# Optimization experiments

Hardware: AMD Instinct MI355X
Metric: run time of the kernel (lower is better)

The kernel has to match this reference:

```python
import jax, jax.numpy as jnp
import numpy as np

B, C, H, N = 4, 128, 4, 2048
D = C // H  # head_dim = 32
BN_EPS = 1e-5


def _conv1(w, b, x):
    # 1x1 Conv1d: [O,C] x [B,C,N] -> [B,O,N]
    return jnp.einsum('oc,bcn->bon', w, x) + b[None, :, None]


def setup_inputs() -> dict:
    key = jax.random.key(0)
    ks = jax.random.split(key, 20)
    p = lambda k, shape: jax.random.normal(k, shape, dtype=jnp.float32) * 0.05
    return {
        'x1': jax.random.normal(ks[0], (B, C, N), dtype=jnp.float32),
        'x2': jax.random.normal(ks[1], (B, C, N), dtype=jnp.float32),
        'kv_mask': jnp.ones((B, N), dtype=bool),
        'wq': p(ks[2], (C, C)), 'bq': p(ks[3], (C,)),
        'wk': p(ks[4], (C, C)), 'bk': p(ks[5], (C,)),
        'wv': p(ks[6], (C, C)), 'bv': p(ks[7], (C,)),
        'wm': p(ks[8], (C, C)), 'bm': p(ks[9], (C,)),
        'wc1': p(ks[10], (2 * C, 2 * C)), 'bc1': p(ks[11], (2 * C,)),
        'bn_gamma': jnp.ones((2 * C,), dtype=jnp.float32),
        'bn_beta': jnp.zeros((2 * C,), dtype=jnp.float32),
        'bn_mean': p(ks[12], (2 * C,)),
        'bn_var': jax.random.uniform(ks[13], (2 * C,), dtype=jnp.float32, minval=0.5, maxval=1.5),
        'wc2': p(ks[14], (C, 2 * C)), 'bc2': p(ks[15], (C,)),
    }


def reference(x1, x2, kv_mask, wq, bq, wk, bk, wv, bv, wm, bm,
              wc1, bc1, bn_gamma, bn_beta, bn_mean, bn_var, wc2, bc2):
    b, _, n = x1.shape
    q = _conv1(wq, bq, x1).reshape(b, H, D, n)   # bhdn
    k = _conv1(wk, bk, x2).reshape(b, H, D, -1)  # bhdm
    v = _conv1(wv, bv, x2).reshape(b, H, D, -1)  # bhdm
    qk = jnp.einsum('bhdn,bhdm->bhnm', q, k)
    # masked_fill on raw QK before scaling, matching torch code
    qk = jnp.where(kv_mask[:, None, None, :], qk, jnp.float32(-1e6))
    score = jax.nn.softmax(qk * (1.0 / D ** 0.5), axis=-1)
    add_value = jnp.einsum('bhnm,bhdm->bhdn', score, v).reshape(b, C, n)
    add_value = _conv1(wm, bm, add_value)
    cat = jnp.concatenate([x1, add_value], axis=1)  # [B, 2C, N]
    h = _conv1(wc1, bc1, cat)
    # BatchNorm1d in inference mode (running stats)
    h = (h - bn_mean[None, :, None]) * jax.lax.rsqrt(bn_var[None, :, None] + BN_EPS)
    h = h * bn_gamma[None, :, None] + bn_beta[None, :, None]
    h = jax.nn.relu(h)
    h = _conv1(wc2, bc2, h)
    return x1 + h
```

## Files before the change

### kernel.cpp

```cpp
#include <hip/hip_runtime.h>

typedef __attribute__((ext_vector_type(4))) float v4f;
typedef __attribute__((ext_vector_type(8))) _Float16 half8;
typedef __attribute__((ext_vector_type(4))) _Float16 half4;
typedef __attribute__((ext_vector_type(2))) _Float16 half2t;

constexpr float C2 = 0.17677669529663687f * 1.44269504088896341f;

__device__ __forceinline__ half4 pk4(float a, float b, float c, float d) {
  half2t lo = __builtin_bit_cast(half2t, __builtin_amdgcn_cvt_pkrtz(a, b));
  half2t hi = __builtin_bit_cast(half2t, __builtin_amdgcn_cvt_pkrtz(c, d));
  return __builtin_shufflevector(lo, hi, 0, 1, 2, 3);
}

__global__ __launch_bounds__(256) void prep(
    const float* __restrict__ x1, const float* __restrict__ x2,
    const float* __restrict__ wq, const float* __restrict__ bq,
    const float* __restrict__ wk, const float* __restrict__ wv,
    const float* __restrict__ wm, const float* __restrict__ wc1,
    const float* __restrict__ wc2, const float* __restrict__ gamma,
    const float* __restrict__ beta, const float* __restrict__ mean,
    const float* __restrict__ var, const unsigned char* __restrict__ mask,
    _Float16* __restrict__ x1pk, _Float16* __restrict__ x2pk,
    _Float16* __restrict__ wts, float* __restrict__ bqs,
    float* __restrict__ A1, float* __restrict__ B1,
    float* __restrict__ maskf) {
  const int id = blockIdx.x * 256 + threadIdx.x;
  if (id < 524288) {
    const int u = id & 262143;
    const float* __restrict__ src = (id < 262144) ? x1 : x2;
    _Float16* __restrict__ dst = (id < 262144) ? x1pk : x2pk;
    const int n = u & 2047, r = u >> 11;
    const int q = r & 3, ct = (r >> 2) & 7, b = r >> 5;
    const float* s = src + ((size_t)(b * 128 + ct * 16 + q * 4) * 2048 + n);
    const half4 v = pk4(s[0], s[2048], s[4096], s[6144]);
    *(half4*)(dst + ((size_t)(b * 8 + ct) * 2048 + n) * 16 + q * 4) = v;
  } else if (id < 565248) {
    const int e = (id - 524288) * 4;
    const float* src;
    int base;
    float sc = 1.0f;
    if (e < 16384) { src = wq; base = 0; sc = C2; }
    else if (e < 32768) { src = wk; base = 16384; }
    else if (e < 49152) { src = wv; base = 32768; }
    else if (e < 65536) { src = wm; base = 49152; }
    else if (e < 131072) { src = wc1; base = 65536; }
    else { src = wc2; base = 131072; }
    const float4 t = *(const float4*)(src + (e - base));
    *(half4*)(wts + e) = pk4(t.x * sc, t.y * sc, t.z * sc, t.w * sc);
  } else if (id < 565312) {
    const int i = (id - 565248) * 4;
#pragma unroll
    for (int j = 0; j < 4; ++j) {
      const int oi = i + j;
      const float sc = gamma[oi] * rsqrtf(var[oi] + 1e-5f);
      A1[oi] = sc;
      B1[oi] = beta[oi] - mean[oi] * sc;
    }
  } else if (id < 565344) {
    const int i = (id - 565312) * 4;
#pragma unroll
    for (int j = 0; j < 4; ++j) bqs[i + j] = bq[i + j] * C2;
  } else if (id < 567392) {
    const int i = (id - 565344) * 4;
#pragma unroll
    for (int j = 0; j < 4; ++j)
      maskf[i + j] = mask[i + j] ? 0.0f : (-1.0e6f * C2);
  }
}

__global__ __launch_bounds__(512) void qkv(
    const _Float16* __restrict__ x1pk, const _Float16* __restrict__ x2pk,
    const _Float16* __restrict__ wts, const float* __restrict__ bqs,
    const float* __restrict__ bk, const float* __restrict__ bv,
    _Float16* __restrict__ Qpk, _Float16* __restrict__ Kpk,
    _Float16* __restrict__ Vpk) {
  const int b = blockIdx.y;
  const int bx = blockIdx.x;
  const int tid = threadIdx.x, w = tid >> 6, lane = tid & 63;
  const int l = lane & 15, q = lane >> 4;
  const int n = bx * 16 + l;
  const size_t xoff = ((size_t)(b * 8 + (q >> 1)) * 2048 + n) * 16 + (q & 1) * 8;

  half8 x1f[4], x2f[4];
#pragma unroll
  for (int kt = 0; kt < 4; ++kt) {
    x1f[kt] = *(const half8*)(x1pk + xoff + (size_t)kt * 2 * 2048 * 16);
    x2f[kt] = *(const half8*)(x2pk + xoff + (size_t)kt * 2 * 2048 * 16);
  }
  const _Float16* wq_h = wts;
  const _Float16* wk_h = wts + 16384;
  const _Float16* wv_h = wts + 32768;

#pragma unroll
  for (int i = 0; i < 3; ++i) {
    const int t = w * 3 + i;
    if (t < 8) {
      const int mt = t;
      v4f acc = *(const v4f*)(bqs + mt * 16 + q * 4);
#pragma unroll
      for (int kt = 0; kt < 4; ++kt) {
        const half8 wf =
            *(const half8*)(wq_h + (mt * 16 + l) * 128 + kt * 32 + q * 8);
        acc = __builtin_amdgcn_mfma_f32_16x16x32_f16(wf, x1f[kt], acc, 0, 0, 0);
      }
      *(half4*)(Qpk + ((size_t)(b * 8 + mt) * 2048 + n) * 16 + q * 4) =
          pk4(acc[0], acc[1], acc[2], acc[3]);
    } else if (t < 16) {
      const int mt = t - 8;
      v4f acc = *(const v4f*)(bk + mt * 16 + q * 4);
#pragma unroll
      for (int kt = 0; kt < 4; ++kt) {
        const half8 wf =
            *(const half8*)(wk_h + (mt * 16 + l) * 128 + kt * 32 + q * 8);
        acc = __builtin_amdgcn_mfma_f32_16x16x32_f16(wf, x2f[kt], acc, 0, 0, 0);
      }
      *(half4*)(Kpk + ((size_t)(b * 8 + mt) * 2048 + n) * 16 + q * 4) =
          pk4(acc[0], acc[1], acc[2], acc[3]);
    } else {
      const int ot = t - 16;
      const float bvv = bv[ot * 16 + l];
      v4f acc = {bvv, bvv, bvv, bvv};
#pragma unroll
      for (int kt = 0; kt < 4; ++kt) {
        const half8 wf =
            *(const half8*)(wv_h + (ot * 16 + l) * 128 + kt * 32 + q * 8);
        acc = __builtin_amdgcn_mfma_f32_16x16x32_f16(x2f[kt], wf, acc, 0, 0, 0);
      }
      *(half4*)(Vpk + (((size_t)(b * 4 + (ot >> 1)) * 128 + bx) * 32 +
                       (ot & 1) * 16 + l) * 16 + q * 4) =
          pk4(acc[0], acc[1], acc[2], acc[3]);
    }
  }
}

__global__ __launch_bounds__(256) void attn(
    const _Float16* __restrict__ Qpk, const _Float16* __restrict__ Kpk,
    const _Float16* __restrict__ Vpk, const float* __restrict__ maskf,
    _Float16* __restrict__ Opk, float* __restrict__ lsump) {
  const int bh = blockIdx.y, b = bh >> 2, h = bh & 3;
  const int n0 = blockIdx.x * 64;
  const int part = blockIdx.z;
  const int tid = threadIdx.x, w = tid >> 6, lane = tid & 63;
  const int l = lane & 15, q = lane >> 4;
  const int n = n0 + w * 16 + l;

  const half8 qf = *(const half8*)(
      Qpk + ((size_t)(b * 8 + h * 2 + (q >> 1)) * 2048 + n) * 16 + (q & 1) * 8);
  const _Float16* __restrict__ Kb =
      Kpk + ((size_t)(b * 8 + h * 2 + (q >> 1)) * 2048) * 16 + (q & 1) * 8;
  const _Float16* __restrict__ Vb =
      Vpk + ((size_t)(b * 4 + h) * 128) * 512 + (size_t)l * 16 + q * 4;
  const float* __restrict__ mf = maskf + b * 2048;

  v4f oacc[2] = {{0.f, 0.f, 0.f, 0.f}, {0.f, 0.f, 0.f, 0.f}};
  float lsum = 0.f;

  const int mbeg = part * 1024;
  for (int m0 = mbeg; m0 < mbeg + 1024; m0 += 64) {
    v4f s[4];
#pragma unroll
    for (int mt = 0; mt < 4; ++mt) {
      const half8 kf = *(const half8*)(Kb + (size_t)(m0 + mt * 16 + l) * 16);
      const v4f biasv = *(const v4f*)(mf + m0 + mt * 16 + q * 4);
      s[mt] = __builtin_amdgcn_mfma_f32_16x16x32_f16(kf, qf, biasv, 0, 0, 0);
    }
    half4 pB[4];
#pragma unroll
    for (int mt = 0; mt < 4; ++mt) {
      const float p0 = exp2f(s[mt][0]), p1 = exp2f(s[mt][1]);
      const float p2 = exp2f(s[mt][2]), p3 = exp2f(s[mt][3]);
      lsum += (p0 + p1) + (p2 + p3);
      pB[mt] = pk4(p0, p1, p2, p3);
    }
#pragma unroll
    for (int mt = 0; mt < 4; ++mt) {
      const size_t vbase = (size_t)((m0 >> 4) + mt) * 512;
#pragma unroll
      for (int df = 0; df < 2; ++df) {
        const half4 vf = *(const half4*)(Vb + vbase + df * 256);
        oacc[df] =
            __builtin_amdgcn_mfma_f32_16x16x16f16(vf, pB[mt], oacc[df], 0, 0, 0);
      }
    }
  }
  lsum += __shfl_xor(lsum, 16);
  lsum += __shfl_xor(lsum, 32);
  if (q == 0) lsump[part * 32768 + bh * 2048 + n] = lsum;
#pragma unroll
  for (int df = 0; df < 2; ++df)
    *(half4*)(Opk + (size_t)part * 1048576 +
              ((size_t)(b * 8 + h * 2 + df) * 2048 + n) * 16 + q * 4) =
        pk4(oacc[df][0], oacc[df][1], oacc[df][2], oacc[df][3]);
}

__global__ __launch_bounds__(512) void post(
    const float* __restrict__ x1, const _Float16* __restrict__ Opk,
    const float* __restrict__ lsump, const _Float16* __restrict__ wts,
    const float* __restrict__ bm, const float* __restrict__ bc1,
    const float* __restrict__ A1, const float* __restrict__ B1,
    const float* __restrict__ bc2, float* __restrict__ out) {
  const int b = blockIdx.y;
  const int n0 = blockIdx.x * 16;
  const int tid = threadIdx.x, w = tid >> 6, lane = tid & 63;
  const int l = lane & 15, q = lane >> 4;
  const int n = n0 + l;
  const _Float16* wm_h = wts + 49152;
  const _Float16* wc1_h = wts + 65536;
  const _Float16* wc2_h = wts + 131072;

  __shared__ _Float16 exA[8 * 256];
  __shared__ _Float16 exB[16 * 256];

  float rlh[4];
#pragma unroll
  for (int hh = 0; hh < 4; ++hh) {
    const size_t idx = (size_t)(b * 4 + hh) * 2048 + n;
    rlh[hh] = 1.0f / (lsump[idx] + lsump[32768 + idx]);
  }
  half4 of[8];
#pragma unroll
  for (int kt = 0; kt < 8; ++kt) {
    const size_t oa = ((size_t)(b * 8 + kt) * 2048 + n) * 16 + q * 4;
    const half4 a = *(const half4*)(Opk + oa);
    const half4 c = *(const half4*)(Opk + 1048576 + oa);
    const _Float16 rh = (_Float16)rlh[kt >> 1];
    const half4 rl4 = {rh, rh, rh, rh};
    of[kt] = (a + c) * rl4;
  }
  half4 catf[16];
  float xr[4];
#pragma unroll
  for (int kt = 0; kt < 8; ++kt) {
    float v0 = x1[(size_t)(b * 128 + kt * 16 + q * 4 + 0) * 2048 + n];
    float v1 = x1[(size_t)(b * 128 + kt * 16 + q * 4 + 1) * 2048 + n];
    float v2 = x1[(size_t)(b * 128 + kt * 16 + q * 4 + 2) * 2048 + n];
    float v3 = x1[(size_t)(b * 128 + kt * 16 + q * 4 + 3) * 2048 + n];
    if (kt == w) { xr[0] = v0; xr[1] = v1; xr[2] = v2; xr[3] = v3; }
    catf[kt] = pk4(v0, v1, v2, v3);
  }
  {
    v4f acc = *(const v4f*)(bm + w * 16 + q * 4);
#pragma unroll
    for (int kt = 0; kt < 8; ++kt) {
      const half4 wf =
          *(const half4*)(wm_h + (w * 16 + l) * 128 + kt * 16 + q * 4);
      acc = __builtin_amdgcn_mfma_f32_16x16x16f16(wf, of[kt], acc, 0, 0, 0);
    }
    *(half4*)&exA[w * 256 + l * 16 + q * 4] = pk4(acc[0], acc[1], acc[2], acc[3]);
  }
  __syncthreads();
#pragma unroll
  for (int f = 0; f < 8; ++f)
    catf[8 + f] = *(const half4*)&exA[f * 256 + l * 16 + q * 4];
#pragma unroll
  for (int i = 0; i < 2; ++i) {
    const int mt = w * 2 + i;
    v4f acc = *(const v4f*)(bc1 + mt * 16 + q * 4);
#pragma unroll
    for (int kt = 0; kt < 16; ++kt) {
      const half4 wf =
          *(const half4*)(wc1_h + (mt * 16 + l) * 256 + kt * 16 + q * 4);
      acc = __builtin_amdgcn_mfma_f32_16x16x16f16(wf, catf[kt], acc, 0, 0, 0);
    }
    const v4f a1 = *(const v4f*)(A1 + mt * 16 + q * 4);
    const v4f b1 = *(const v4f*)(B1 + mt * 16 + q * 4);
    const float h0 = fmaxf(acc[0] * a1[0] + b1[0], 0.f);
    const float h1 = fmaxf(acc[1] * a1[1] + b1[1], 0.f);
    const float h2 = fmaxf(acc[2] * a1[2] + b1[2], 0.f);
    const float h3 = fmaxf(acc[3] * a1[3] + b1[3], 0.f);
    *(half4*)&exB[mt * 256 + l * 16 + q * 4] = pk4(h0, h1, h2, h3);
  }
  __syncthreads();
  {
    v4f acc = *(const v4f*)(bc2 + w * 16 + q * 4);
#pragma unroll
    for (int kt = 0; kt < 16; ++kt) {
      const half4 hfv = *(const half4*)&exB[kt * 256 + l * 16 + q * 4];
      const half4 wf =
          *(const half4*)(wc2_h + (w * 16 + l) * 256 + kt * 16 + q * 4);
      acc = __builtin_amdgcn_mfma_f32_16x16x16f16(wf, hfv, acc, 0, 0, 0);
    }
#pragma unroll
    for (int r = 0; r < 4; ++r)
      out[(size_t)(b * 128 + w * 16 + q * 4 + r) * 2048 + n] = acc[r] + xr[r];
  }
}

extern "C" void kernel_launch(void* const* d_in, const int* in_sizes, int n_in,
                              void* d_out, int out_size, void* d_ws,
                              size_t ws_size, hipStream_t stream) {
  const float* x1 = (const float*)d_in[0];
  const float* x2 = (const float*)d_in[1];
  const unsigned char* kv_mask = (const unsigned char*)d_in[2];
  const float* wq = (const float*)d_in[3];
  const float* bq = (const float*)d_in[4];
  const float* wk = (const float*)d_in[5];
  const float* bk = (const float*)d_in[6];
  const float* wv = (const float*)d_in[7];
  const float* bv = (const float*)d_in[8];
  const float* wm = (const float*)d_in[9];
  const float* bm = (const float*)d_in[10];
  const float* wc1 = (const float*)d_in[11];
  const float* bc1 = (const float*)d_in[12];
  const float* bn_gamma = (const float*)d_in[13];
  const float* bn_beta = (const float*)d_in[14];
  const float* bn_mean = (const float*)d_in[15];
  const float* bn_var = (const float*)d_in[16];
  const float* wc2 = (const float*)d_in[17];
  const float* bc2 = (const float*)d_in[18];
  float* out = (float*)d_out;

  char* p = (char*)d_ws;
  _Float16* x1pk = (_Float16*)p;
  _Float16* x2pk = (_Float16*)(p + (size_t)2 * 1024 * 1024);
  _Float16* Qpk = (_Float16*)(p + (size_t)4 * 1024 * 1024);
  _Float16* Kpk = (_Float16*)(p + (size_t)6 * 1024 * 1024);
  _Float16* Vpk = (_Float16*)(p + (size_t)8 * 1024 * 1024);
  _Float16* Opk = (_Float16*)(p + (size_t)10 * 1024 * 1024);
  _Float16* wts = (_Float16*)(p + (size_t)14 * 1024 * 1024);
  float* lsump = (float*)(p + (size_t)14 * 1024 * 1024 + 512 * 1024);
  float* maskf = lsump + 65536;
  float* bqs = maskf + 8192;
  float* A1 = bqs + 128;
  float* B1 = A1 + 256;

  prep<<<2217, 256, 0, stream>>>(x1, x2, wq, bq, wk, wv, wm, wc1, wc2,
                                 bn_gamma, bn_beta, bn_mean, bn_var, kv_mask,
                                 x1pk, x2pk, wts, bqs, A1, B1, maskf);
  qkv<<<dim3(128, 4), 512, 0, stream>>>(x1pk, x2pk, wts, bqs, bk, bv, Qpk, Kpk,
                                        Vpk);
  attn<<<dim3(32, 16, 2), 256, 0, stream>>>(Qpk, Kpk, Vpk, maskf, Opk, lsump);
  post<<<dim3(128, 4), 512, 0, stream>>>(x1, Opk, lsump, wts, bm, bc1, A1, B1,
                                         bc2, out);
}
```

Baseline: 168.5 us.

## Fuse prep into qkv, reshape attention tiling with four key splits

Removes the separate prep kernel. The qkv kernel now loads fp32 x1/x2 and the Q/K/V weights directly and converts them to fp16 in registers, while a few blocks also pack the post-stage weights and the mask bias. Attention now gives each wave two 16-query tiles that share every K/V load, and splits the key range into four partitions instead of two, so the post kernel sums four partial outputs and row sums. BatchNorm scale and shift are computed inline in post. In exchange, the QKV weight conversion is repeated in every block, and the extra partial results add memory traffic.

Result: no change. 170.4 us (+1.1%).

```diff
diff --git a/kernel.cpp b/kernel.cpp
--- a/kernel.cpp
+++ b/kernel.cpp
@@ -12,108 +12,83 @@
   half2t hi = __builtin_bit_cast(half2t, __builtin_amdgcn_cvt_pkrtz(c, d));
   return __builtin_shufflevector(lo, hi, 0, 1, 2, 3);
 }
-
-__global__ __launch_bounds__(256) void prep(
+__device__ __forceinline__ half8 pk8f4(const float4 a, const float4 b) {
+  const half4 lo = pk4(a.x, a.y, a.z, a.w);
+  const half4 hi = pk4(b.x, b.y, b.z, b.w);
+  return __builtin_shufflevector(lo, hi, 0, 1, 2, 3, 4, 5, 6, 7);
+}
+
+__global__ __launch_bounds__(512) void qkv(
     const float* __restrict__ x1, const float* __restrict__ x2,
     const float* __restrict__ wq, const float* __restrict__ bq,
-    const float* __restrict__ wk, const float* __restrict__ wv,
+    const float* __restrict__ wk, const float* __restrict__ bk,
+    const float* __restrict__ wv, const float* __restrict__ bv,
     const float* __restrict__ wm, const float* __restrict__ wc1,
-    const float* __restrict__ wc2, const float* __restrict__ gamma,
-    const float* __restrict__ beta, const float* __restrict__ mean,
-    const float* __restrict__ var, const unsigned char* __restrict__ mask,
-    _Float16* __restrict__ x1pk, _Float16* __restrict__ x2pk,
-    _Float16* __restrict__ wts, float* __restrict__ bqs,
-    float* __restrict__ A1, float* __restrict__ B1,
+    const float* __restrict__ wc2, const unsigned char* __restrict__ mask,
+    _Float16* __restrict__ Qpk, _Float16* __restrict__ Kpk,
+    _Float16* __restrict__ Vpk, _Float16* __restrict__ wts,
     float* __restrict__ maskf) {
-  const int id = blockIdx.x * 256 + threadIdx.x;
-  if (id < 524288) {
-    const int u = id & 262143;
-    const float* __restrict__ src = (id < 262144) ? x1 : x2;
-    _Float16* __restrict__ dst = (id < 262144) ? x1pk : x2pk;
-    const int n = u & 2047, r = u >> 11;
-    const int q = r & 3, ct = (r >> 2) & 7, b = r >> 5;
-    const float* s = src + ((size_t)(b * 128 + ct * 16 + q * 4) * 2048 + n);
-    const half4 v = pk4(s[0], s[2048], s[4096], s[6144]);
-    *(half4*)(dst + ((size_t)(b * 8 + ct) * 2048 + n) * 16 + q * 4) = v;
-  } else if (id < 565248) {
-    const int e = (id - 524288) * 4;
-    const float* src;
-    int base;
-    float sc = 1.0f;
-    if (e < 16384) { src = wq; base = 0; sc = C2; }
-    else if (e < 32768) { src = wk; base = 16384; }
-    else if (e < 49152) { src = wv; base = 32768; }
-    else if (e < 65536) { src = wm; base = 49152; }
-    else if (e < 131072) { src = wc1; base = 65536; }
-    else { src = wc2; base = 131072; }
-    const float4 t = *(const float4*)(src + (e - base));
-    *(half4*)(wts + e) = pk4(t.x * sc, t.y * sc, t.z * sc, t.w * sc);
-  } else if (id < 565312) {
-    const int i = (id - 565248) * 4;
-#pragma unroll
-    for (int j = 0; j < 4; ++j) {
-      const int oi = i + j;
-      const float sc = gamma[oi] * rsqrtf(var[oi] + 1e-5f);
-      A1[oi] = sc;
-      B1[oi] = beta[oi] - mean[oi] * sc;
-    }
-  } else if (id < 565344) {
-    const int i = (id - 565312) * 4;
-#pragma unroll
-    for (int j = 0; j < 4; ++j) bqs[i + j] = bq[i + j] * C2;
-  } else if (id < 567392) {
-    const int i = (id - 565344) * 4;
-#pragma unroll
-    for (int j = 0; j < 4; ++j)
-      maskf[i + j] = mask[i + j] ? 0.0f : (-1.0e6f * C2);
-  }
-}
-
-__global__ __launch_bounds__(512) void qkv(
-    const _Float16* __restrict__ x1pk, const _Float16* __restrict__ x2pk,
-    const _Float16* __restrict__ wts, const float* __restrict__ bqs,
-    const float* __restrict__ bk, const float* __restrict__ bv,
-    _Float16* __restrict__ Qpk, _Float16* __restrict__ Kpk,
-    _Float16* __restrict__ Vpk) {
   const int b = blockIdx.y;
   const int bx = blockIdx.x;
   const int tid = threadIdx.x, w = tid >> 6, lane = tid & 63;
   const int l = lane & 15, q = lane >> 4;
   const int n = bx * 16 + l;
-  const size_t xoff = ((size_t)(b * 8 + (q >> 1)) * 2048 + n) * 16 + (q & 1) * 8;
+
+  if (b == 0 && bx < 72) {
+    const int e = (bx * 512 + tid) * 4;
+    const float* src;
+    int base;
+    if (e < 16384) { src = wm; base = 0; }
+    else if (e < 81920) { src = wc1; base = 16384; }
+    else { src = wc2; base = 81920; }
+    const float4 t = *(const float4*)(src + (e - base));
+    *(half4*)(wts + e) = pk4(t.x, t.y, t.z, t.w);
+  } else if (b == 1 && bx < 4) {
+    const int e = (bx * 512 + tid) * 4;
+    const unsigned mv = *(const unsigned*)(mask + e);
+    float4 o;
+    o.x = (mv & 0x000000ffu) ? 0.f : -1.0e6f * C2;
+    o.y = (mv & 0x0000ff00u) ? 0.f : -1.0e6f * C2;
+    o.z = (mv & 0x00ff0000u) ? 0.f : -1.0e6f * C2;
+    o.w = (mv & 0xff000000u) ? 0.f : -1.0e6f * C2;
+    *(float4*)(maskf + e) = o;
+  }
 
   half8 x1f[4], x2f[4];
 #pragma unroll
   for (int kt = 0; kt < 4; ++kt) {
-    x1f[kt] = *(const half8*)(x1pk + xoff + (size_t)kt * 2 * 2048 * 16);
-    x2f[kt] = *(const half8*)(x2pk + xoff + (size_t)kt * 2 * 2048 * 16);
-  }
-  const _Float16* wq_h = wts;
-  const _Float16* wk_h = wts + 16384;
-  const _Float16* wv_h = wts + 32768;
+    float4 a, c;
+    const size_t rb = (size_t)(b * 128 + kt * 32 + q * 8) * 2048 + n;
+    a.x = x1[rb]; a.y = x1[rb + 2048]; a.z = x1[rb + 4096]; a.w = x1[rb + 6144];
+    c.x = x1[rb + 8192]; c.y = x1[rb + 10240]; c.z = x1[rb + 12288]; c.w = x1[rb + 14336];
+    x1f[kt] = pk8f4(a, c);
+    a.x = x2[rb]; a.y = x2[rb + 2048]; a.z = x2[rb + 4096]; a.w = x2[rb + 6144];
+    c.x = x2[rb + 8192]; c.y = x2[rb + 10240]; c.z = x2[rb + 12288]; c.w = x2[rb + 14336];
+    x2f[kt] = pk8f4(a, c);
+  }
 
 #pragma unroll
   for (int i = 0; i < 3; ++i) {
     const int t = w * 3 + i;
     if (t < 8) {
       const int mt = t;
-      v4f acc = *(const v4f*)(bqs + mt * 16 + q * 4);
+      v4f acc = *(const v4f*)(bq + mt * 16 + q * 4);
 #pragma unroll
       for (int kt = 0; kt < 4; ++kt) {
-        const half8 wf =
-            *(const half8*)(wq_h + (mt * 16 + l) * 128 + kt * 32 + q * 8);
-        acc = __builtin_amdgcn_mfma_f32_16x16x32_f16(wf, x1f[kt], acc, 0, 0, 0);
+        const float4 wa = *(const float4*)(wq + (mt * 16 + l) * 128 + kt * 32 + q * 8);
+        const float4 wb = *(const float4*)(wq + (mt * 16 + l) * 128 + kt * 32 + q * 8 + 4);
+        acc = __builtin_amdgcn_mfma_f32_16x16x32_f16(pk8f4(wa, wb), x1f[kt], acc, 0, 0, 0);
       }
       *(half4*)(Qpk + ((size_t)(b * 8 + mt) * 2048 + n) * 16 + q * 4) =
-          pk4(acc[0], acc[1], acc[2], acc[3]);
+          pk4(acc[0] * C2, acc[1] * C2, acc[2] * C2, acc[3] * C2);
     } else if (t < 16) {
       const int mt = t - 8;
       v4f acc = *(const v4f*)(bk + mt * 16 + q * 4);
 #pragma unroll
       for (int kt = 0; kt < 4; ++kt) {
-        const half8 wf =
-            *(const half8*)(wk_h + (mt * 16 + l) * 128 + kt * 32 + q * 8);
-        acc = __builtin_amdgcn_mfma_f32_16x16x32_f16(wf, x2f[kt], acc, 0, 0, 0);
+        const float4 wa = *(const float4*)(wk + (mt * 16 + l) * 128 + kt * 32 + q * 8);
+        const float4 wb = *(const float4*)(wk + (mt * 16 + l) * 128 + kt * 32 + q * 8 + 4);
+        acc = __builtin_amdgcn_mfma_f32_16x16x32_f16(pk8f4(wa, wb), x2f[kt], acc, 0, 0, 0);
       }
       *(half4*)(Kpk + ((size_t)(b * 8 + mt) * 2048 + n) * 16 + q * 4) =
           pk4(acc[0], acc[1], acc[2], acc[3]);
@@ -123,9 +98,9 @@
       v4f acc = {bvv, bvv, bvv, bvv};
 #pragma unroll
       for (int kt = 0; kt < 4; ++kt) {
-        const half8 wf =
-            *(const half8*)(wv_h + (ot * 16 + l) * 128 + kt * 32 + q * 8);
-        acc = __builtin_amdgcn_mfma_f32_16x16x32_f16(x2f[kt], wf, acc, 0, 0, 0);
+        const float4 wa = *(const float4*)(wv + (ot * 16 + l) * 128 + kt * 32 + q * 8);
+        const float4 wb = *(const float4*)(wv + (ot * 16 + l) * 128 + kt * 32 + q * 8 + 4);
+        acc = __builtin_amdgcn_mfma_f32_16x16x32_f16(x2f[kt], pk8f4(wa, wb), acc, 0, 0, 0);
       }
       *(half4*)(Vpk + (((size_t)(b * 4 + (ot >> 1)) * 128 + bx) * 32 +
                        (ot & 1) * 16 + l) * 16 + q * 4) =
@@ -139,75 +114,85 @@
     const _Float16* __restrict__ Vpk, const float* __restrict__ maskf,
     _Float16* __restrict__ Opk, float* __restrict__ lsump) {
   const int bh = blockIdx.y, b = bh >> 2, h = bh & 3;
-  const int n0 = blockIdx.x * 64;
   const int part = blockIdx.z;
   const int tid = threadIdx.x, w = tid >> 6, lane = tid & 63;
   const int l = lane & 15, q = lane >> 4;
-  const int n = n0 + w * 16 + l;
-
-  const half8 qf = *(const half8*)(
-      Qpk + ((size_t)(b * 8 + h * 2 + (q >> 1)) * 2048 + n) * 16 + (q & 1) * 8);
-  const _Float16* __restrict__ Kb =
-      Kpk + ((size_t)(b * 8 + h * 2 + (q >> 1)) * 2048) * 16 + (q & 1) * 8;
+  const int nb = blockIdx.x * 128 + w * 32;
+
+  const size_t qrow = (size_t)(b * 8 + h * 2 + (q >> 1)) * 2048;
+  const half8 qf0 = *(const half8*)(Qpk + (qrow + nb + l) * 16 + (q & 1) * 8);
+  const half8 qf1 = *(const half8*)(Qpk + (qrow + nb + 16 + l) * 16 + (q & 1) * 8);
+  const _Float16* __restrict__ Kb = Kpk + qrow * 16 + (q & 1) * 8;
   const _Float16* __restrict__ Vb =
       Vpk + ((size_t)(b * 4 + h) * 128) * 512 + (size_t)l * 16 + q * 4;
   const float* __restrict__ mf = maskf + b * 2048;
 
-  v4f oacc[2] = {{0.f, 0.f, 0.f, 0.f}, {0.f, 0.f, 0.f, 0.f}};
-  float lsum = 0.f;
-
-  const int mbeg = part * 1024;
-  for (int m0 = mbeg; m0 < mbeg + 1024; m0 += 64) {
-    v4f s[4];
+  v4f oacc[2][2] = {{{0.f, 0.f, 0.f, 0.f}, {0.f, 0.f, 0.f, 0.f}},
+                    {{0.f, 0.f, 0.f, 0.f}, {0.f, 0.f, 0.f, 0.f}}};
+  float ls0 = 0.f, ls1 = 0.f;
+
+  const int mbeg = part * 512;
+  for (int m0 = mbeg; m0 < mbeg + 512; m0 += 64) {
+    half4 pB[2][4];
 #pragma unroll
     for (int mt = 0; mt < 4; ++mt) {
       const half8 kf = *(const half8*)(Kb + (size_t)(m0 + mt * 16 + l) * 16);
       const v4f biasv = *(const v4f*)(mf + m0 + mt * 16 + q * 4);
-      s[mt] = __builtin_amdgcn_mfma_f32_16x16x32_f16(kf, qf, biasv, 0, 0, 0);
-    }
-    half4 pB[4];
-#pragma unroll
-    for (int mt = 0; mt < 4; ++mt) {
-      const float p0 = exp2f(s[mt][0]), p1 = exp2f(s[mt][1]);
-      const float p2 = exp2f(s[mt][2]), p3 = exp2f(s[mt][3]);
-      lsum += (p0 + p1) + (p2 + p3);
-      pB[mt] = pk4(p0, p1, p2, p3);
+      const v4f s0 = __builtin_amdgcn_mfma_f32_16x16x32_f16(kf, qf0, biasv, 0, 0, 0);
+      const v4f s1 = __builtin_amdgcn_mfma_f32_16x16x32_f16(kf, qf1, biasv, 0, 0, 0);
+      const float a0 = exp2f(s0[0]), a1 = exp2f(s0[1]), a2 = exp2f(s0[2]),
+                  a3 = exp2f(s0[3]);
+      const float c0 = exp2f(s1[0]), c1 = exp2f(s1[1]), c2 = exp2f(s1[2]),
+                  c3 = exp2f(s1[3]);
+      ls0 += (a0 + a1) + (a2 + a3);
+      ls1 += (c0 + c1) + (c2 + c3);
+      pB[0][mt] = pk4(a0, a1, a2, a3);
+      pB[1][mt] = pk4(c0, c1, c2, c3);
     }
 #pragma unroll
     for (int mt = 0; mt < 4; ++mt) {
       const size_t vbase = (size_t)((m0 >> 4) + mt) * 512;
-#pragma unroll
-      for (int df = 0; df < 2; ++df) {
-        const half4 vf = *(const half4*)(Vb + vbase + df * 256);
-        oacc[df] =
-            __builtin_amdgcn_mfma_f32_16x16x16f16(vf, pB[mt], oacc[df], 0, 0, 0);
-      }
-    }
-  }
-  lsum += __shfl_xor(lsum, 16);
-  lsum += __shfl_xor(lsum, 32);
-  if (q == 0) lsump[part * 32768 + bh * 2048 + n] = lsum;
-#pragma unroll
-  for (int df = 0; df < 2; ++df)
-    *(half4*)(Opk + (size_t)part * 1048576 +
-              ((size_t)(b * 8 + h * 2 + df) * 2048 + n) * 16 + q * 4) =
-        pk4(oacc[df][0], oacc[df][1], oacc[df][2], oacc[df][3]);
+      const half4 vf0 = *(const half4*)(Vb + vbase);
+      const half4 vf1 = *(const half4*)(Vb + vbase + 256);
+      oacc[0][0] = __builtin_amdgcn_mfma_f32_16x16x16f16(vf0, pB[0][mt], oacc[0][0], 0, 0, 0);
+      oacc[0][1] = __builtin_amdgcn_mfma_f32_16x16x16f16(vf1, pB[0][mt], oacc[0][1], 0, 0, 0);
+      oacc[1][0] = __builtin_amdgcn_mfma_f32_16x16x16f16(vf0, pB[1][mt], oacc[1][0], 0, 0, 0);
+      oacc[1][1] = __builtin_amdgcn_mfma_f32_16x16x16f16(vf1, pB[1][mt], oacc[1][1], 0, 0, 0);
+    }
+  }
+  ls0 += __shfl_xor(ls0, 16);
+  ls0 += __shfl_xor(ls0, 32);
+  ls1 += __shfl_xor(ls1, 16);
+  ls1 += __shfl_xor(ls1, 32);
+  if (q == 0) {
+    lsump[part * 32768 + bh * 2048 + nb + l] = ls0;
+    lsump[part * 32768 + bh * 2048 + nb + 16 + l] = ls1;
+  }
+#pragma unroll
+  for (int qt = 0; qt < 2; ++qt)
+#pragma unroll
+    for (int df = 0; df < 2; ++df)
+      *(half4*)(Opk + (size_t)part * 1048576 +
+                ((size_t)(b * 8 + h * 2 + df) * 2048 + nb + qt * 16 + l) * 16 +
+                q * 4) = pk4(oacc[qt][df][0], oacc[qt][df][1], oacc[qt][df][2],
+                             oacc[qt][df][3]);
 }
 
 __global__ __launch_bounds__(512) void post(
     const float* __restrict__ x1, const _Float16* __restrict__ Opk,
     const float* __restrict__ lsump, const _Float16* __restrict__ wts,
     const float* __restrict__ bm, const float* __restrict__ bc1,
-    const float* __restrict__ A1, const float* __restrict__ B1,
+    const float* __restrict__ gamma, const float* __restrict__ beta,
+    const float* __restrict__ mean, const float* __restrict__ var,
     const float* __restrict__ bc2, float* __restrict__ out) {
   const int b = blockIdx.y;
   const int n0 = blockIdx.x * 16;
   const int tid = threadIdx.x, w = tid >> 6, lane = tid & 63;
   const int l = lane & 15, q = lane >> 4;
   const int n = n0 + l;
-  const _Float16* wm_h = wts + 49152;
-  const _Float16* wc1_h = wts + 65536;
-  const _Float16* wc2_h = wts + 131072;
+  const _Float16* wm_h = wts;
+  const _Float16* wc1_h = wts + 16384;
+  const _Float16* wc2_h = wts + 81920;
 
   __shared__ _Float16 exA[8 * 256];
   __shared__ _Float16 exB[16 * 256];
@@ -216,7 +201,8 @@
 #pragma unroll
   for (int hh = 0; hh < 4; ++hh) {
     const size_t idx = (size_t)(b * 4 + hh) * 2048 + n;
-    rlh[hh] = 1.0f / (lsump[idx] + lsump[32768 + idx]);
+    rlh[hh] = 1.0f / (lsump[idx] + lsump[32768 + idx] + lsump[65536 + idx] +
+                      lsump[98304 + idx]);
   }
   half4 of[8];
 #pragma unroll
@@ -224,18 +210,20 @@
     const size_t oa = ((size_t)(b * 8 + kt) * 2048 + n) * 16 + q * 4;
     const half4 a = *(const half4*)(Opk + oa);
     const half4 c = *(const half4*)(Opk + 1048576 + oa);
+    const half4 d = *(const half4*)(Opk + 2097152 + oa);
+    const half4 e = *(const half4*)(Opk + 3145728 + oa);
     const _Float16 rh = (_Float16)rlh[kt >> 1];
     const half4 rl4 = {rh, rh, rh, rh};
-    of[kt] = (a + c) * rl4;
+    of[kt] = ((a + c) + (d + e)) * rl4;
   }
   half4 catf[16];
   float xr[4];
 #pragma unroll
   for (int kt = 0; kt < 8; ++kt) {
-    float v0 = x1[(size_t)(b * 128 + kt * 16 + q * 4 + 0) * 2048 + n];
-    float v1 = x1[(size_t)(b * 128 + kt * 16 + q * 4 + 1) * 2048 + n];
-    float v2 = x1[(size_t)(b * 128 + kt * 16 + q * 4 + 2) * 2048 + n];
-    float v3 = x1[(size_t)(b * 128 + kt * 16 + q * 4 + 3) * 2048 + n];
+    const float v0 = x1[(size_t)(b * 128 + kt * 16 + q * 4 + 0) * 2048 + n];
+    const float v1 = x1[(size_t)(b * 128 + kt * 16 + q * 4 + 1) * 2048 + n];
+    const float v2 = x1[(size_t)(b * 128 + kt * 16 + q * 4 + 2) * 2048 + n];
+    const float v3 = x1[(size_t)(b * 128 + kt * 16 + q * 4 + 3) * 2048 + n];
     if (kt == w) { xr[0] = v0; xr[1] = v1; xr[2] = v2; xr[3] = v3; }
     catf[kt] = pk4(v0, v1, v2, v3);
   }
@@ -243,8 +231,7 @@
     v4f acc = *(const v4f*)(bm + w * 16 + q * 4);
 #pragma unroll
     for (int kt = 0; kt < 8; ++kt) {
-      const half4 wf =
-          *(const half4*)(wm_h + (w * 16 + l) * 128 + kt * 16 + q * 4);
+      const half4 wf = *(const half4*)(wm_h + (w * 16 + l) * 128 + kt * 16 + q * 4);
       acc = __builtin_amdgcn_mfma_f32_16x16x16f16(wf, of[kt], acc, 0, 0, 0);
     }
     *(half4*)&exA[w * 256 + l * 16 + q * 4] = pk4(acc[0], acc[1], acc[2], acc[3]);
@@ -259,17 +246,21 @@
     v4f acc = *(const v4f*)(bc1 + mt * 16 + q * 4);
 #pragma unroll
     for (int kt = 0; kt < 16; ++kt) {
-      const half4 wf =
-          *(const half4*)(wc1_h + (mt * 16 + l) * 256 + kt * 16 + q * 4);
+      const half4 wf = *(const half4*)(wc1_h + (mt * 16 + l) * 256 + kt * 16 + q * 4);
       acc = __builtin_amdgcn_mfma_f32_16x16x16f16(wf, catf[kt], acc, 0, 0, 0);
     }
-    const v4f a1 = *(const v4f*)(A1 + mt * 16 + q * 4);
-    const v4f b1 = *(const v4f*)(B1 + mt * 16 + q * 4);
-    const float h0 = fmaxf(acc[0] * a1[0] + b1[0], 0.f);
-    const float h1 = fmaxf(acc[1] * a1[1] + b1[1], 0.f);
-    const float h2 = fmaxf(acc[2] * a1[2] + b1[2], 0.f);
-    const float h3 = fmaxf(acc[3] * a1[3] + b1[3], 0.f);
-    *(half4*)&exB[mt * 256 + l * 16 + q * 4] = pk4(h0, h1, h2, h3);
+    const v4f g = *(const v4f*)(gamma + mt * 16 + q * 4);
+    const v4f bt = *(const v4f*)(beta + mt * 16 + q * 4);
+    const v4f mn = *(const v4f*)(mean + mt * 16 + q * 4);
+    const v4f vr = *(const v4f*)(var + mt * 16 + q * 4);
+    float hh[4];
+#pragma unroll
+    for (int r = 0; r < 4; ++r) {
+      const float a1 = g[r] * rsqrtf(vr[r] + 1e-5f);
+      const float b1 = bt[r] - mn[r] * a1;
+      hh[r] = fmaxf(acc[r] * a1 + b1, 0.f);
+    }
+    *(half4*)&exB[mt * 256 + l * 16 + q * 4] = pk4(hh[0], hh[1], hh[2], hh[3]);
   }
   __syncthreads();
   {
@@ -277,8 +268,7 @@
 #pragma unroll
     for (int kt = 0; kt < 16; ++kt) {
       const half4 hfv = *(const half4*)&exB[kt * 256 + l * 16 + q * 4];
-      const half4 wf =
-          *(const half4*)(wc2_h + (w * 16 + l) * 256 + kt * 16 + q * 4);
+      const half4 wf = *(const half4*)(wc2_h + (w * 16 + l) * 256 + kt * 16 + q * 4);
       acc = __builtin_amdgcn_mfma_f32_16x16x16f16(wf, hfv, acc, 0, 0, 0);
     }
 #pragma unroll
@@ -312,25 +302,19 @@
   float* out = (float*)d_out;
 
   char* p = (char*)d_ws;
-  _Float16* x1pk = (_Float16*)p;
-  _Float16* x2pk = (_Float16*)(p + (size_t)2 * 1024 * 1024);
-  _Float16* Qpk = (_Float16*)(p + (size_t)4 * 1024 * 1024);
-  _Float16* Kpk = (_Float16*)(p + (size_t)6 * 1024 * 1024);
-  _Float16* Vpk = (_Float16*)(p + (size_t)8 * 1024 * 1024);
-  _Float16* Opk = (_Float16*)(p + (size_t)10 * 1024 * 1024);
+  _Float16* Qpk = (_Float16*)p;
+  _Float16* Kpk = (_Float16*)(p + (size_t)2 * 1024 * 1024);
+  _Float16* Vpk = (_Float16*)(p + (size_t)4 * 1024 * 1024);
+  _Float16* Opk = (_Float16*)(p + (size_t)6 * 1024 * 1024);
   _Float16* wts = (_Float16*)(p + (size_t)14 * 1024 * 1024);
   float* lsump = (float*)(p + (size_t)14 * 1024 * 1024 + 512 * 1024);
-  float* maskf = lsump + 65536;
-  float* bqs = maskf + 8192;
-  float* A1 = bqs + 128;
-  float* B1 = A1 + 256;
-
-  prep<<<2217, 256, 0, stream>>>(x1, x2, wq, bq, wk, wv, wm, wc1, wc2,
-                                 bn_gamma, bn_beta, bn_mean, bn_var, kv_mask,
-                                 x1pk, x2pk, wts, bqs, A1, B1, maskf);
-  qkv<<<dim3(128, 4), 512, 0, stream>>>(x1pk, x2pk, wts, bqs, bk, bv, Qpk, Kpk,
-                                        Vpk);
-  attn<<<dim3(32, 16, 2), 256, 0, stream>>>(Qpk, Kpk, Vpk, maskf, Opk, lsump);
-  post<<<dim3(128, 4), 512, 0, stream>>>(x1, Opk, lsump, wts, bm, bc1, A1, B1,
+  float* maskf = lsump + 4 * 32768;
+
+  qkv<<<dim3(128, 4), 512, 0, stream>>>(x1, x2, wq, bq, wk, bk, wv, bv, wm,
+                                        wc1, wc2, kv_mask, Qpk, Kpk, Vpk, wts,
+                                        maskf);
+  attn<<<dim3(16, 16, 4), 256, 0, stream>>>(Qpk, Kpk, Vpk, maskf, Opk, lsump);
+  post<<<dim3(128, 4), 512, 0, stream>>>(x1, Opk, lsump, wts, bm, bc1,
+                                         bn_gamma, bn_beta, bn_mean, bn_var,
                                          bc2, out);
 }
```
